# Kernel tuning notes

Measured on AMD Instinct MI355X. Metric: run time of the kernel, lower is better.

## Reference

```python
import jax, jax.numpy as jnp
import numpy as np

N_NODES = 50000


def _inv_sqrt_deg(idx, n):
    # degree per node from an edge-endpoint index vector; 0-degree -> norm 0 (DGL behavior)
    deg = jax.ops.segment_sum(jnp.ones(idx.shape[0], jnp.float32), idx, num_segments=n)
    return jnp.where(deg > 0, jax.lax.rsqrt(jnp.maximum(deg, 1.0)), 0.0)


def _graph_conv(x, src, dst, W, b, norm_src, norm_dst, n):
    # DGL GraphConv, norm='both': D_dst^{-1/2} A D_src^{-1/2} X W + b
    h = (x * norm_src[:, None]) @ W            # [N, out]
    agg = jax.ops.segment_sum(h[src], dst, num_segments=n)  # SpMM via gather+scatter-add
    return agg * norm_dst[:, None] + b


def setup_inputs() -> dict:
    key = jax.random.key(0)
    ks = jax.random.split(key, 8)
    N, E, D, H, C = N_NODES, 800000, 64, 64, 10
    s = 1.0 / np.sqrt(H)
    return {
        "x": jax.random.normal(ks[0], (N, D), jnp.float32),
        "src": jax.random.randint(ks[1], (E,), 0, N, jnp.int32),
        "dst": jax.random.randint(ks[2], (E,), 0, N, jnp.int32),
        "W1": jax.random.normal(ks[3], (D, H), jnp.float32) * s,
        "b1": jnp.zeros((H,), jnp.float32),
        "W2": jax.random.normal(ks[4], (H, H), jnp.float32) * s,
        "b2": jnp.zeros((H,), jnp.float32),
        "W3": jax.random.normal(ks[5], (H, H), jnp.float32) * s,
        "b3": jnp.zeros((H,), jnp.float32),
        "Wfc": jax.random.normal(ks[6], (H, C), jnp.float32) * s,
        "bfc": jnp.zeros((C,), jnp.float32),
    }


def reference(x, src, dst, W1, b1, W2, b2, W3, b3, Wfc, bfc):
    n = x.shape[0]
    norm_src = _inv_sqrt_deg(src, n)  # out-degree^{-1/2}
    norm_dst = _inv_sqrt_deg(dst, n)  # in-degree^{-1/2}
    h = jnp.tanh(_graph_conv(x, src, dst, W1, b1, norm_src, norm_dst, n))
    h = jnp.tanh(_graph_conv(h, src, dst, W2, b2, norm_src, norm_dst, n))
    h = jnp.tanh(_graph_conv(h, src, dst, W3, b3, norm_src, norm_dst, n))
    return h @ Wfc + bfc
```

## Files before the change

kernel.cpp:

```cpp
#include <hip/hip_runtime.h>
#include <hip/hip_fp16.h>
#include <math.h>

#define THREADS 256
#define CHUNK_SHIFT 14
#define CHUNK (1 << CHUNK_SHIFT)
#define LDS_WORDS 12500
#define MAXB 16
#define XS_STRIDE 68

__global__ __launch_bounds__(1024)
void k_hist(const int* __restrict__ src, const int* __restrict__ dst,
            unsigned int* __restrict__ partS, unsigned int* __restrict__ partD,
            unsigned char* __restrict__ rank, unsigned int* __restrict__ counter,
            int E, int P, int words) {
    __shared__ unsigned int hist[LDS_WORDS];
    if (blockIdx.x == 0 && threadIdx.x == 0) *counter = 0u;
    int isSrc = (blockIdx.x >= (unsigned)P);
    int b = isSrc ? (blockIdx.x - P) : blockIdx.x;
    int tid = threadIdx.x;

    for (int w = tid; w < words; w += 1024) hist[w] = 0u;
    __syncthreads();

    int start = b << CHUNK_SHIFT;
    int end = start + CHUNK; if (end > E) end = E;

    if (isSrc) {
        for (int e = start + tid; e < end; e += 1024) {
            int s = src[e];
            atomicAdd(&hist[s >> 2], 1u << ((s & 3) * 8));
        }
    } else {
        for (int e = start + tid; e < end; e += 1024) {
            int d = dst[e];
            unsigned int old = atomicAdd(&hist[d >> 2], 1u << ((d & 3) * 8));
            rank[e] = (unsigned char)((old >> ((d & 3) * 8)) & 0xFFu);
        }
    }
    __syncthreads();

    unsigned int* part = isSrc ? partS : partD;
    for (int w = tid; w < words; w += 1024)
        part[(size_t)b * words + w] = hist[w];
}

__global__ __launch_bounds__(THREADS)
void k_pre(const unsigned int* __restrict__ partS,
           const unsigned int* __restrict__ partD,
           unsigned int* __restrict__ prefD,
           int* __restrict__ deg_d, float* __restrict__ ns, float* __restrict__ nd,
           int* __restrict__ rp, int* __restrict__ bsum,
           unsigned int* __restrict__ counter,
           int P, int words, int N) {
    __shared__ unsigned int qsD[4][64];
    __shared__ unsigned int qsS[4][64];
    int t = threadIdx.x;
    int widx = t & 63;
    int q = t >> 6;
    int w = blockIdx.x * 64 + widx;
    bool valid = (w < words);

    int per = (P + 3) >> 2;
    int blo = q * per;
    int cnt = P - blo; if (cnt > per) cnt = per; if (cnt < 0) cnt = 0;

    unsigned int vD[MAXB];
    unsigned int runD = 0, runS = 0;
#pragma unroll
    for (int bb = 0; bb < MAXB; bb++) {
        unsigned int vd = 0, vs = 0;
        if (bb < cnt && valid) {
            size_t off = (size_t)(blo + bb) * words + w;
            vd = partD[off];
            vs = partS[off];
        }
        vD[bb] = vd;
        runD += vd;
        runS += vs;
    }
    qsD[q][widx] = runD;
    qsS[q][widx] = runS;
    __syncthreads();

    unsigned int baseD = 0, totD = 0, totS = 0;
#pragma unroll
    for (int qq = 0; qq < 4; qq++) {
        unsigned int xd = qsD[qq][widx];
        unsigned int xs = qsS[qq][widx];
        if (qq < q) baseD += xd;
        totD += xd;
        totS += xs;
    }

    unsigned int pref = baseD;
#pragma unroll
    for (int bb = 0; bb < MAXB; bb++) {
        if (bb < cnt && valid)
            prefD[(size_t)(blo + bb) * words + w] = pref;
        pref += vD[bb];
    }

    if (q == 0) {
        int b0 = (int)(totD & 0xFFu), b1 = (int)((totD >> 8) & 0xFFu),
            b2 = (int)((totD >> 16) & 0xFFu), b3 = (int)((totD >> 24) & 0xFFu);
        int wsum = b0 + b1 + b2 + b3;
        int incl = wsum;
#pragma unroll
        for (int off = 1; off < 64; off <<= 1) {
            int y = __shfl_up(incl, off);
            if (widx >= off) incl += y;
        }
        int excl = incl - wsum;
        int btot = __shfl(incl, 63);
        if (widx == 0)
            bsum[blockIdx.x] = (int)atomicAdd(counter, (unsigned int)btot);
        if (valid) {
            int s0 = (int)(totS & 0xFFu), s1 = (int)((totS >> 8) & 0xFFu),
                s2 = (int)((totS >> 16) & 0xFFu), s3 = (int)((totS >> 24) & 0xFFu);
            int4 dv; dv.x = b0; dv.y = b1; dv.z = b2; dv.w = b3;
            *(int4*)&deg_d[(size_t)4 * w] = dv;
            float4 ndv;
            ndv.x = b0 ? 1.0f / sqrtf((float)b0) : 0.0f;
            ndv.y = b1 ? 1.0f / sqrtf((float)b1) : 0.0f;
            ndv.z = b2 ? 1.0f / sqrtf((float)b2) : 0.0f;
            ndv.w = b3 ? 1.0f / sqrtf((float)b3) : 0.0f;
            *(float4*)&nd[(size_t)4 * w] = ndv;
            float4 nsv;
            nsv.x = s0 ? 1.0f / sqrtf((float)s0) : 0.0f;
            nsv.y = s1 ? 1.0f / sqrtf((float)s1) : 0.0f;
            nsv.z = s2 ? 1.0f / sqrtf((float)s2) : 0.0f;
            nsv.w = s3 ? 1.0f / sqrtf((float)s3) : 0.0f;
            *(float4*)&ns[(size_t)4 * w] = nsv;
            int4 rv; rv.x = excl; rv.y = excl + b0;
            rv.z = excl + b0 + b1; rv.w = excl + b0 + b1 + b2;
            *(int4*)&rp[(size_t)4 * w] = rv;
        }
    }
}

__global__ __launch_bounds__(256, 4)
void k_fill_gemm(const int* __restrict__ src, const int* __restrict__ dst,
                 const int* __restrict__ rp, const int* __restrict__ bsum,
                 const unsigned char* __restrict__ rank,
                 const unsigned int* __restrict__ prefD,
                 int* __restrict__ col, int E, int words, int gFill,
                 const float* __restrict__ X, const float* __restrict__ norm,
                 const float* __restrict__ W, __half* __restrict__ H, int N) {
    __shared__ float Xs[64 * XS_STRIDE];
    __shared__ float Ws[64 * 64];
    int tid = threadIdx.x;

    if ((int)blockIdx.x < gFill) {
        int e = blockIdx.x * 256 + tid;
        if (e < E) {
            int d = dst[e];
            int b = e >> CHUNK_SHIFT;
            unsigned int pk = prefD[(size_t)b * words + (d >> 2)];
            int pref = (int)((pk >> ((d & 3) * 8)) & 0xFFu);
            col[rp[d] + bsum[d >> 8] + pref + (int)rank[e]] = src[e];
        }
        return;
    }

    int rowBase = ((int)blockIdx.x - gFill) * 64;
    for (int i = tid; i < 1024; i += 256)
        ((float4*)Ws)[i] = ((const float4*)W)[i];
    for (int i = tid; i < 1024; i += 256) {
        int r  = i >> 4;
        int k4 = i & 15;
        int row = rowBase + r;
        float4 v = make_float4(0.f, 0.f, 0.f, 0.f);
        if (row < N) {
            v = ((const float4*)X)[(size_t)row * 16 + k4];
            float nv = norm[row];
            v.x *= nv; v.y *= nv; v.z *= nv; v.w *= nv;
        }
        *((float4*)&Xs[r * XS_STRIDE + (k4 << 2)]) = v;
    }
    __syncthreads();

    int tc = tid & 15;
    int tr = tid >> 4;
    int c0 = tc * 4, r0 = tr * 4;
    float acc[4][4] = {};

#pragma unroll 2
    for (int k = 0; k < 64; k += 4) {
        float4 wv[4];
#pragma unroll
        for (int kk = 0; kk < 4; kk++)
            wv[kk] = *((const float4*)&Ws[(k + kk) * 64 + c0]);
#pragma unroll
        for (int j = 0; j < 4; j++) {
            float4 xv = *((const float4*)&Xs[(r0 + j) * XS_STRIDE + k]);
            acc[j][0] += xv.x * wv[0].x; acc[j][1] += xv.x * wv[0].y;
            acc[j][2] += xv.x * wv[0].z; acc[j][3] += xv.x * wv[0].w;
            acc[j][0] += xv.y * wv[1].x; acc[j][1] += xv.y * wv[1].y;
            acc[j][2] += xv.y * wv[1].z; acc[j][3] += xv.y * wv[1].w;
            acc[j][0] += xv.z * wv[2].x; acc[j][1] += xv.z * wv[2].y;
            acc[j][2] += xv.z * wv[2].z; acc[j][3] += xv.z * wv[2].w;
            acc[j][0] += xv.w * wv[3].x; acc[j][1] += xv.w * wv[3].y;
            acc[j][2] += xv.w * wv[3].z; acc[j][3] += xv.w * wv[3].w;
        }
    }
#pragma unroll
    for (int j = 0; j < 4; j++) {
        int row = rowBase + r0 + j;
        if (row < N) {
            __half2 h01 = __floats2half2_rn(acc[j][0], acc[j][1]);
            __half2 h23 = __floats2half2_rn(acc[j][2], acc[j][3]);
            uint2 pk;
            pk.x = *(unsigned int*)&h01;
            pk.y = *(unsigned int*)&h23;
            *((uint2*)(H + (size_t)row * 64 + c0)) = pk;
        }
    }
}

template<int FC>
__global__ __launch_bounds__(256, 4)
void k_agg_gemm(const uint4* __restrict__ H4, const int* __restrict__ rp,
                const int* __restrict__ bsum, const int* __restrict__ deg,
                const int* __restrict__ col, const float* __restrict__ nd,
                const float* __restrict__ nsrc, const float* __restrict__ bias,
                const float* __restrict__ W, const float* __restrict__ Wb2,
                void* __restrict__ OutP, int N) {
    __shared__ float Xs[64 * XS_STRIDE];
    __shared__ float Ws[FC ? 640 : 4096];
    __shared__ float Wb[16];
    int tid = threadIdx.x;

    if constexpr (FC == 0) {
        for (int i = tid; i < 1024; i += 256)
            ((float4*)Ws)[i] = ((const float4*)W)[i];
    } else {
        for (int i = tid; i < 640; i += 256) {
            int k = i / 10, c = i - k * 10;
            Ws[c * 64 + k] = W[i];
        }
        if (tid < 10) Wb[tid] = Wb2[tid];
    }

    int wave = tid >> 6;
    int lane = tid & 63;
    int g = lane >> 3;
    int l = lane & 7;
    int g0 = (lane >> 3) & 1, g1 = (lane >> 4) & 1, g2 = (lane >> 5) & 1;
    int ch = (l << 3) + (g0 << 2) + (g1 << 1) + g2;
    float bv = bias[ch];
    int rowBase = blockIdx.x * 64;

    int node = rowBase + wave * 16;
    int start = 0, n = 0;
    float nv = 0.f, nsv = 0.f;
    if (node < N) {
        start = rp[node] + bsum[node >> 8];
        n = deg[node];
        nv = nd[node];
        if constexpr (FC == 0) nsv = nsrc[node];
    }

#pragma unroll 1
    for (int i = 0; i < 16; i++) {
        int nextNode = node + 1;
        int nStart = 0, nN = 0;
        float nNv = 0.f, nNs = 0.f;
        if (i < 15 && nextNode < N) {
            nStart = rp[nextNode] + bsum[nextNode >> 8];
            nN = deg[nextNode];
            nNv = nd[nextNode];
            if constexpr (FC == 0) nNs = nsrc[nextNode];
        }

        int sStart = __builtin_amdgcn_readfirstlane(start);
        int sN     = __builtin_amdgcn_readfirstlane(n);
        float a[8] = {0.f, 0.f, 0.f, 0.f, 0.f, 0.f, 0.f, 0.f};

        auto accum = [&](uint4 v) {
            float2 f0 = __half22float2(*(__half2*)&v.x);
            float2 f1 = __half22float2(*(__half2*)&v.y);
            float2 f2 = __half22float2(*(__half2*)&v.z);
            float2 f3 = __half22float2(*(__half2*)&v.w);
            a[0] += f0.x; a[1] += f0.y; a[2] += f1.x; a[3] += f1.y;
            a[4] += f2.x; a[5] += f2.y; a[6] += f3.x; a[7] += f3.y;
        };

        if (sN <= 32) {
            int idx = (lane < sN) ? col[sStart + lane] : 0;
            int s0 = __shfl(idx, g);
            uint4 z; z.x = 0u; z.y = 0u; z.z = 0u; z.w = 0u;
            uint4 v0 = z, v1 = z, v2 = z, v3 = z;
            if (g < sN) v0 = H4[(size_t)s0 * 8 + l];
            if (sN > 8) {
                int s1 = __shfl(idx, 8 + g);
                if (8 + g < sN) v1 = H4[(size_t)s1 * 8 + l];
            }
            if (sN > 16) {
                int s2 = __shfl(idx, 16 + g);
                if (16 + g < sN) v2 = H4[(size_t)s2 * 8 + l];
            }
            if (sN > 24) {
                int s3 = __shfl(idx, 24 + g);
                if (24 + g < sN) v3 = H4[(size_t)s3 * 8 + l];
            }
            accum(v0);
            if (sN > 8)  accum(v1);
            if (sN > 16) accum(v2);
            if (sN > 24) accum(v3);
        } else {
            for (int base = 0; base < sN; base += 64) {
                int cnt = sN - base;
                if (cnt > 64) cnt = 64;
                int idx = (lane < cnt) ? col[sStart + base + lane] : 0;
                int j = 0;
                for (; j + 32 <= cnt; j += 32) {
                    int s0 = __shfl(idx, j + g);
                    int s1 = __shfl(idx, j + 8 + g);
                    int s2 = __shfl(idx, j + 16 + g);
                    int s3 = __shfl(idx, j + 24 + g);
                    uint4 v0 = H4[(size_t)s0 * 8 + l];
                    uint4 v1 = H4[(size_t)s1 * 8 + l];
                    uint4 v2 = H4[(size_t)s2 * 8 + l];
                    uint4 v3 = H4[(size_t)s3 * 8 + l];
                    accum(v0); accum(v1); accum(v2); accum(v3);
                }
                for (; j + 8 <= cnt; j += 8) {
                    int s0 = __shfl(idx, j + g);
                    uint4 v0 = H4[(size_t)s0 * 8 + l];
                    accum(v0);
                }
                int tl = cnt - j;
                if (tl > 0) {
                    int s0 = __shfl(idx, j + (g < tl ? g : 0));
                    if (g < tl) {
                        uint4 v0 = H4[(size_t)s0 * 8 + l];
                        accum(v0);
                    }
                }
            }
        }

        float b_[4];
#pragma unroll
        for (int j = 0; j < 4; j++) {
            float send = g0 ? a[j] : a[j + 4];
            float recv = __shfl_xor(send, 8);
            float keep = g0 ? a[j + 4] : a[j];
            b_[j] = keep + recv;
        }
        float c_[2];
#pragma unroll
        for (int j = 0; j < 2; j++) {
            float send = g1 ? b_[j] : b_[j + 2];
            float recv = __shfl_xor(send, 16);
            float keep = g1 ? b_[j + 2] : b_[j];
            c_[j] = keep + recv;
        }
        float send = g2 ? c_[0] : c_[1];
        float recv = __shfl_xor(send, 32);
        float keep = g2 ? c_[1] : c_[0];
        float s = keep + recv;

        float tv = tanhf(s * nv + bv);
        float val;
        if constexpr (FC == 0) val = tv * nsv;
        else                   val = tv;
        Xs[(wave * 16 + i) * XS_STRIDE + ch] = (node < N) ? val : 0.0f;

        node = nextNode; start = nStart; n = nN; nv = nNv; nsv = nNs;
    }
    __syncthreads();

    if constexpr (FC == 0) {
        __half* Hh = (__half*)OutP;
        int tc = tid & 15;
        int tr = tid >> 4;
        int c0 = tc * 4, r0 = tr * 4;
        float acc[4][4] = {};

#pragma unroll 2
        for (int k = 0; k < 64; k += 4) {
            float4 wv[4];
#pragma unroll
            for (int kk = 0; kk < 4; kk++)
                wv[kk] = *((const float4*)&Ws[(k + kk) * 64 + c0]);
#pragma unroll
            for (int j = 0; j < 4; j++) {
                float4 xv = *((const float4*)&Xs[(r0 + j) * XS_STRIDE + k]);
                acc[j][0] += xv.x * wv[0].x; acc[j][1] += xv.x * wv[0].y;
                acc[j][2] += xv.x * wv[0].z; acc[j][3] += xv.x * wv[0].w;
                acc[j][0] += xv.y * wv[1].x; acc[j][1] += xv.y * wv[1].y;
                acc[j][2] += xv.y * wv[1].z; acc[j][3] += xv.y * wv[1].w;
                acc[j][0] += xv.z * wv[2].x; acc[j][1] += xv.z * wv[2].y;
                acc[j][2] += xv.z * wv[2].z; acc[j][3] += xv.z * wv[2].w;
                acc[j][0] += xv.w * wv[3].x; acc[j][1] += xv.w * wv[3].y;
                acc[j][2] += xv.w * wv[3].z; acc[j][3] += xv.w * wv[3].w;
            }
        }
#pragma unroll
        for (int j = 0; j < 4; j++) {
            int row = rowBase + r0 + j;
            if (row < N) {
                __half2 h01 = __floats2half2_rn(acc[j][0], acc[j][1]);
                __half2 h23 = __floats2half2_rn(acc[j][2], acc[j][3]);
                uint2 pk;
                pk.x = *(unsigned int*)&h01;
                pk.y = *(unsigned int*)&h23;
                *((uint2*)(Hh + (size_t)row * 64 + c0)) = pk;
            }
        }
    } else {
        float* outF = (float*)OutP;
        for (int idx = tid; idx < 640; idx += 256) {
            int ln = idx / 10;
            int cl = idx - ln * 10;
            float acc = Wb[cl];
#pragma unroll
            for (int k = 0; k < 64; k += 4) {
                float4 xv = *((const float4*)&Xs[ln * XS_STRIDE + k]);
                float4 wv = *((const float4*)&Ws[cl * 64 + k]);
                acc += xv.x * wv.x;
                acc += xv.y * wv.y;
                acc += xv.z * wv.z;
                acc += xv.w * wv.w;
            }
            int row = rowBase + ln;
            if (row < N) outF[(size_t)row * 10 + cl] = acc;
        }
    }
}

extern "C" void kernel_launch(void* const* d_in, const int* in_sizes, int n_in,
                              void* d_out, int out_size, void* d_ws, size_t ws_size,
                              hipStream_t stream) {
    const float* x   = (const float*)d_in[0];
    const int*   src = (const int*)d_in[1];
    const int*   dst = (const int*)d_in[2];
    const float* W1  = (const float*)d_in[3];
    const float* b1  = (const float*)d_in[4];
    const float* W2  = (const float*)d_in[5];
    const float* b2  = (const float*)d_in[6];
    const float* W3  = (const float*)d_in[7];
    const float* b3  = (const float*)d_in[8];
    const float* Wfc = (const float*)d_in[9];
    const float* bfc = (const float*)d_in[10];
    float* out = (float*)d_out;
    int N = in_sizes[0] / 64;
    int E = in_sizes[1];
    int P = (E + CHUNK - 1) >> CHUNK_SHIFT;
    int words = (N + 3) / 4;

    char* ws = (char*)d_ws;
    size_t p = 0;
    auto alloc = [&](size_t bytes) -> void* {
        void* r = ws + p;
        p = (p + bytes + 255) & ~(size_t)255;
        return r;
    };
    int*    deg_d = (int*)alloc((size_t)N * 4);
    int*    rp    = (int*)alloc((size_t)N * 4);
    int*    bsum  = (int*)alloc((size_t)THREADS * 4);
    unsigned char* rank = (unsigned char*)alloc((size_t)E);
    int*    col   = (int*)alloc((size_t)E * 4);
    float*  ns    = (float*)alloc((size_t)N * 4);
    float*  nd    = (float*)alloc((size_t)N * 4);
    unsigned int* partS = (unsigned int*)alloc((size_t)P * words * 4);
    unsigned int* partD = (unsigned int*)alloc((size_t)P * words * 4);
    unsigned int* prefD = (unsigned int*)alloc((size_t)P * words * 4);
    __half* bufH  = (__half*)alloc((size_t)N * 64 * 2);
    __half* bufH2 = (__half*)alloc((size_t)N * 64 * 2);
    unsigned int* counter = (unsigned int*)alloc(4);
    (void)ws_size; (void)n_in; (void)out_size;

    int gFill = (E + 255) / 256;
    int gP = (words + 63) / 64;
    int gG = (N + 63) / 64;

    k_hist<<<2 * P, 1024, 0, stream>>>(src, dst, partS, partD, rank, counter, E, P, words);
    k_pre <<<gP, THREADS, 0, stream>>>(partS, partD, prefD, deg_d, ns, nd,
                                       rp, bsum, counter, P, words, N);
    k_fill_gemm<<<gFill + gG, 256, 0, stream>>>(src, dst, rp, bsum, rank, prefD,
                                                col, E, words, gFill,
                                                x, ns, W1, bufH, N);
    k_agg_gemm<0><<<gG, 256, 0, stream>>>((const uint4*)bufH,  rp, bsum, deg_d, col,
                                          nd, ns, b1, W2, nullptr, bufH2, N);
    k_agg_gemm<0><<<gG, 256, 0, stream>>>((const uint4*)bufH2, rp, bsum, deg_d, col,
                                          nd, ns, b2, W3, nullptr, bufH, N);
    k_agg_gemm<1><<<gG, 256, 0, stream>>>((const uint4*)bufH,  rp, bsum, deg_d, col,
                                          nd, ns, b3, Wfc, bfc, out, N);
}
```

Baseline: 215.3 us.

## Assign one node per 8-lane group in SpMM gather instead of per-wave

The aggregation loop is restructured so each 8-lane group in a wave handles its own destination node (two nodes per group), rather than a whole wave processing one node at a time with a cross-group shuffle reduction. This removes the per-node butterfly reduction and serial node loop, and lets eight nodes' gathers run concurrently per wave. Loop trip count is the wave-wide max degree, so lanes with shorter neighbor lists sit idle under divergence. The histogram chunk size constant is also doubled.

```diff
diff --git a/kernel.cpp b/kernel.cpp
--- a/kernel.cpp
+++ b/kernel.cpp
@@ -3,7 +3,7 @@
 #include <math.h>
 
 #define THREADS 256
-#define CHUNK_SHIFT 14
+#define CHUNK_SHIFT 15
 #define CHUNK (1 << CHUNK_SHIFT)
 #define LDS_WORDS 12500
 #define MAXB 16
@@ -246,130 +246,82 @@
     int lane = tid & 63;
     int g = lane >> 3;
     int l = lane & 7;
-    int g0 = (lane >> 3) & 1, g1 = (lane >> 4) & 1, g2 = (lane >> 5) & 1;
-    int ch = (l << 3) + (g0 << 2) + (g1 << 1) + g2;
-    float bv = bias[ch];
     int rowBase = blockIdx.x * 64;
 
-    int node = rowBase + wave * 16;
-    int start = 0, n = 0;
-    float nv = 0.f, nsv = 0.f;
-    if (node < N) {
-        start = rp[node] + bsum[node >> 8];
-        n = deg[node];
-        nv = nd[node];
-        if constexpr (FC == 0) nsv = nsrc[node];
-    }
-
-#pragma unroll 1
-    for (int i = 0; i < 16; i++) {
-        int nextNode = node + 1;
-        int nStart = 0, nN = 0;
-        float nNv = 0.f, nNs = 0.f;
-        if (i < 15 && nextNode < N) {
-            nStart = rp[nextNode] + bsum[nextNode >> 8];
-            nN = deg[nextNode];
-            nNv = nd[nextNode];
-            if constexpr (FC == 0) nNs = nsrc[nextNode];
-        }
-
-        int sStart = __builtin_amdgcn_readfirstlane(start);
-        int sN     = __builtin_amdgcn_readfirstlane(n);
-        float a[8] = {0.f, 0.f, 0.f, 0.f, 0.f, 0.f, 0.f, 0.f};
-
-        auto accum = [&](uint4 v) {
-            float2 f0 = __half22float2(*(__half2*)&v.x);
-            float2 f1 = __half22float2(*(__half2*)&v.y);
-            float2 f2 = __half22float2(*(__half2*)&v.z);
-            float2 f3 = __half22float2(*(__half2*)&v.w);
-            a[0] += f0.x; a[1] += f0.y; a[2] += f1.x; a[3] += f1.y;
-            a[4] += f2.x; a[5] += f2.y; a[6] += f3.x; a[7] += f3.y;
-        };
-
-        if (sN <= 32) {
-            int idx = (lane < sN) ? col[sStart + lane] : 0;
-            int s0 = __shfl(idx, g);
-            uint4 z; z.x = 0u; z.y = 0u; z.z = 0u; z.w = 0u;
-            uint4 v0 = z, v1 = z, v2 = z, v3 = z;
-            if (g < sN) v0 = H4[(size_t)s0 * 8 + l];
-            if (sN > 8) {
-                int s1 = __shfl(idx, 8 + g);
-                if (8 + g < sN) v1 = H4[(size_t)s1 * 8 + l];
-            }
-            if (sN > 16) {
-                int s2 = __shfl(idx, 16 + g);
-                if (16 + g < sN) v2 = H4[(size_t)s2 * 8 + l];
-            }
-            if (sN > 24) {
-                int s3 = __shfl(idx, 24 + g);
-                if (24 + g < sN) v3 = H4[(size_t)s3 * 8 + l];
-            }
-            accum(v0);
-            if (sN > 8)  accum(v1);
-            if (sN > 16) accum(v2);
-            if (sN > 24) accum(v3);
-        } else {
-            for (int base = 0; base < sN; base += 64) {
-                int cnt = sN - base;
-                if (cnt > 64) cnt = 64;
-                int idx = (lane < cnt) ? col[sStart + base + lane] : 0;
-                int j = 0;
-                for (; j + 32 <= cnt; j += 32) {
-                    int s0 = __shfl(idx, j + g);
-                    int s1 = __shfl(idx, j + 8 + g);
-                    int s2 = __shfl(idx, j + 16 + g);
-                    int s3 = __shfl(idx, j + 24 + g);
-                    uint4 v0 = H4[(size_t)s0 * 8 + l];
-                    uint4 v1 = H4[(size_t)s1 * 8 + l];
-                    uint4 v2 = H4[(size_t)s2 * 8 + l];
-                    uint4 v3 = H4[(size_t)s3 * 8 + l];
-                    accum(v0); accum(v1); accum(v2); accum(v3);
-                }
-                for (; j + 8 <= cnt; j += 8) {
-                    int s0 = __shfl(idx, j + g);
-                    uint4 v0 = H4[(size_t)s0 * 8 + l];
-                    accum(v0);
-                }
-                int tl = cnt - j;
-                if (tl > 0) {
-                    int s0 = __shfl(idx, j + (g < tl ? g : 0));
-                    if (g < tl) {
-                        uint4 v0 = H4[(size_t)s0 * 8 + l];
-                        accum(v0);
-                    }
+    float4 bv0 = *((const float4*)&bias[l * 8]);
+    float4 bv1 = *((const float4*)&bias[l * 8 + 4]);
+
+    int nodeA = rowBase + wave * 16 + g;
+    int nodeB = nodeA + 8;
+
+    int stA = 0, nA = 0; float nvA = 0.f, nsA = 0.f;
+    if (nodeA < N) {
+        stA = rp[nodeA] + bsum[nodeA >> 8];
+        nA  = deg[nodeA];
+        nvA = nd[nodeA];
+        if constexpr (FC == 0) nsA = nsrc[nodeA];
+    }
+    int stB = 0, nB = 0; float nvB = 0.f, nsB = 0.f;
+    if (nodeB < N) {
+        stB = rp[nodeB] + bsum[nodeB >> 8];
+        nB  = deg[nodeB];
+        nvB = nd[nodeB];
+        if constexpr (FC == 0) nsB = nsrc[nodeB];
+    }
+
+    int idxA = (l < nA) ? col[stA + l] : 0;
+    int idxB = (l < nB) ? col[stB + l] : 0;
+
+    int mA = nA, mB = nB;
+#pragma unroll
+    for (int d = 8; d <= 32; d <<= 1) {
+        int tA = __shfl_xor(mA, d); mA = mA > tA ? mA : tA;
+        int tB = __shfl_xor(mB, d); mB = mB > tB ? mB : tB;
+    }
+
+    auto run = [&](int start, int n, int m, int idx, float nv, float nsv,
+                   bool vn, int row) {
+        float acc[8] = {0.f, 0.f, 0.f, 0.f, 0.f, 0.f, 0.f, 0.f};
+        for (int j0 = 0; j0 < m; j0 += 8) {
+            int idxn = ((j0 + 8 + l) < n) ? col[start + j0 + 8 + l] : 0;
+#pragma unroll
+            for (int jj = 0; jj < 8; jj++) {
+                int s = __shfl(idx, (g << 3) + jj);
+                if (j0 + jj < n) {
+                    uint4 v = H4[(size_t)s * 8 + l];
+                    float2 f0 = __half22float2(*(__half2*)&v.x);
+                    float2 f1 = __half22float2(*(__half2*)&v.y);
+                    float2 f2 = __half22float2(*(__half2*)&v.z);
+                    float2 f3 = __half22float2(*(__half2*)&v.w);
+                    acc[0] += f0.x; acc[1] += f0.y; acc[2] += f1.x; acc[3] += f1.y;
+                    acc[4] += f2.x; acc[5] += f2.y; acc[6] += f3.x; acc[7] += f3.y;
                 }
             }
-        }
-
-        float b_[4];
-#pragma unroll
-        for (int j = 0; j < 4; j++) {
-            float send = g0 ? a[j] : a[j + 4];
-            float recv = __shfl_xor(send, 8);
-            float keep = g0 ? a[j + 4] : a[j];
-            b_[j] = keep + recv;
-        }
-        float c_[2];
-#pragma unroll
-        for (int j = 0; j < 2; j++) {
-            float send = g1 ? b_[j] : b_[j + 2];
-            float recv = __shfl_xor(send, 16);
-            float keep = g1 ? b_[j + 2] : b_[j];
-            c_[j] = keep + recv;
-        }
-        float send = g2 ? c_[0] : c_[1];
-        float recv = __shfl_xor(send, 32);
-        float keep = g2 ? c_[1] : c_[0];
-        float s = keep + recv;
-
-        float tv = tanhf(s * nv + bv);
-        float val;
-        if constexpr (FC == 0) val = tv * nsv;
-        else                   val = tv;
-        Xs[(wave * 16 + i) * XS_STRIDE + ch] = (node < N) ? val : 0.0f;
-
-        node = nextNode; start = nStart; n = nN; nv = nNv; nsv = nNs;
-    }
+            idx = idxn;
+        }
+        float4 o0, o1;
+        o0.x = tanhf(acc[0] * nv + bv0.x);
+        o0.y = tanhf(acc[1] * nv + bv0.y);
+        o0.z = tanhf(acc[2] * nv + bv0.z);
+        o0.w = tanhf(acc[3] * nv + bv0.w);
+        o1.x = tanhf(acc[4] * nv + bv1.x);
+        o1.y = tanhf(acc[5] * nv + bv1.y);
+        o1.z = tanhf(acc[6] * nv + bv1.z);
+        o1.w = tanhf(acc[7] * nv + bv1.w);
+        if constexpr (FC == 0) {
+            o0.x *= nsv; o0.y *= nsv; o0.z *= nsv; o0.w *= nsv;
+            o1.x *= nsv; o1.y *= nsv; o1.z *= nsv; o1.w *= nsv;
+        }
+        if (!vn) {
+            o0 = make_float4(0.f, 0.f, 0.f, 0.f);
+            o1 = make_float4(0.f, 0.f, 0.f, 0.f);
+        }
+        *((float4*)&Xs[row * XS_STRIDE + l * 8])     = o0;
+        *((float4*)&Xs[row * XS_STRIDE + l * 8 + 4]) = o1;
+    };
+
+    run(stA, nA, mA, idxA, nvA, nsA, nodeA < N, wave * 16 + g);
+    run(stB, nB, mB, idxB, nvB, nsB, nodeB < N, wave * 16 + 8 + g);
     __syncthreads();
 
     if constexpr (FC == 0) {
```

After: 214.8 us. Within noise of the previous version (-0.2%).
